# Performance work log

Hardware: AMD Instinct MI355X
Metric: run time of the kernel (lower is better)

## Reference

```python
import jax, jax.numpy as jnp
import numpy as np

HEAD_DIM = 256
L2_EPS = 1e-12  # tf.math.l2_normalize default epsilon


def setup_inputs() -> dict:
    key = jax.random.key(0)
    ks = jax.random.split(key, 6)
    B, U = 64, 2048
    D_dec, D_enc = 1024, 512
    H, K, A = 4, HEAD_DIM, 1024
    s = 0.075  # RandomUniform(-0.075, 0.075) kernel init
    return {
        "dec_state": jax.random.normal(ks[0], (B, D_dec), jnp.float32),
        "enc_state": jax.random.normal(ks[1], (B, U, D_enc), jnp.float32),
        "phi_w": jax.random.uniform(ks[2], (H, D_dec, K), jnp.float32, -s, s),
        "phi_b": jnp.zeros((H, K), jnp.float32),
        "psi_w": jax.random.uniform(ks[3], (H, D_enc, K), jnp.float32, -s, s),
        "psi_b": jnp.zeros((H, K), jnp.float32),
        "out_w": jax.random.uniform(ks[4], (H * D_enc, A), jnp.float32, -s, s),
        "out_b": jnp.zeros((A,), jnp.float32),
    }


def reference(dec_state, enc_state, phi_w, phi_b, psi_w, psi_b, out_w, out_b):
    B = dec_state.shape[0]
    # Per-head query/key projections, all heads at once.
    phi_s = jnp.einsum("bd,hdk->bhk", dec_state, phi_w) + phi_b[None]      # (B,H,K)
    psi_h = jnp.einsum("bue,hek->bhuk", enc_state, psi_w) + psi_b[None, :, None]  # (B,H,U,K)
    scale = 1.0 / jnp.sqrt(jnp.asarray(HEAD_DIM, jnp.float32))
    energy = jnp.einsum("bhk,bhuk->bhu", phi_s, psi_h) * scale              # (B,H,U)
    attn = jax.nn.softmax(energy, axis=-1)
    # NOTE: the original attends over the RAW enc_state (not psi_h).
    ctx = jnp.einsum("bhu,bue->bhe", attn, enc_state)                        # (B,H,E)
    # tf.math.l2_normalize over last axis
    sq = jnp.sum(ctx * ctx, axis=-1, keepdims=True)
    ctx = ctx * jax.lax.rsqrt(jnp.maximum(sq, L2_EPS))
    combined = ctx.reshape(B, -1)                                            # (B, H*E) == concat over heads
    return combined @ out_w + out_b
```

## Files before the change

kernel.cpp:

```cpp
#include <hip/hip_runtime.h>
#include <math.h>

typedef float f2 __attribute__((ext_vector_type(2)));

constexpr int NB = 64;
constexpr int NU = 2048;
constexpr int ND = 1024;
constexpr int NE = 512;
constexpr int NH = 4;
constexpr int NK = 256;
constexpr int NA = 1024;
constexpr int NS = 16;
constexpr int ROWS_PER_BLOCK = NU / NS;
constexpr int ROWS_PER_WAVE  = ROWS_PER_BLOCK / 4;
constexpr float SCALE = 0.0625f;

constexpr int RSPLIT = 16;
constexpr int RCH = (NH*NE)/RSPLIT;
constexpr int BT = 8;

constexpr int DSP = 16;

constexpr size_t WS_Q   = 0;
constexpr size_t WS_CTX = WS_Q + (size_t)NB*NH*NE;
constexpr size_t WS_P   = WS_CTX + (size_t)NB*NH*NE;

__global__ __launch_bounds__(256) void k_phi(
    const float* __restrict__ dec, const float* __restrict__ phi_w,
    float* __restrict__ P, float* __restrict__ q, float* __restrict__ ctxacc,
    const float* __restrict__ out_b, float* __restrict__ out)
{
  const int flat = blockIdx.x;
  const int kc = flat & 3;
  const int h  = (flat >> 2) & 3;
  const int ds = flat >> 4;
  const int t = threadIdx.x;

  ctxacc[(size_t)flat*512 + t]       = 0.f;
  ctxacc[(size_t)flat*512 + 256 + t] = 0.f;
  q[(size_t)flat*512 + t]            = 0.f;
  q[(size_t)flat*512 + 256 + t]      = 0.f;
  out[(size_t)flat*256 + t] = out_b[(flat*256 + t) & (NA-1)];

  const int d0 = ds*64, k0 = kc*64;

  __shared__ float phi_lds[64][64];
  __shared__ float dec_t[64][68];

  {
    const int kq = t & 15, r = t >> 4;
    const float* pwb = phi_w + ((size_t)h*ND + d0)*NK + k0;
    #pragma unroll
    for (int p = 0; p < 4; ++p) {
      float4 v = *(const float4*)(pwb + (size_t)(r + 16*p)*NK + 4*kq);
      *(float4*)&phi_lds[r + 16*p][4*kq] = v;
    }
    const float* db = dec + d0 + 4*kq;
    #pragma unroll
    for (int p = 0; p < 4; ++p) {
      const int b = r + 16*p;
      float4 v = *(const float4*)(db + (size_t)b*ND);
      dec_t[4*kq+0][b] = v.x; dec_t[4*kq+1][b] = v.y;
      dec_t[4*kq+2][b] = v.z; dec_t[4*kq+3][b] = v.w;
    }
  }
  __syncthreads();

  const int k = t & 63, bq = t >> 6, b0 = bq*16;
  f2 acc2[8];
  #pragma unroll
  for (int i = 0; i < 8; ++i) acc2[i] = f2{0.f, 0.f};
  #pragma unroll 4
  for (int d = 0; d < 64; ++d) {
    float w = phi_lds[d][k];
    f2 ww = f2{w, w};
    float4 a0 = *(const float4*)&dec_t[d][b0];
    float4 a1 = *(const float4*)&dec_t[d][b0+4];
    float4 a2 = *(const float4*)&dec_t[d][b0+8];
    float4 a3 = *(const float4*)&dec_t[d][b0+12];
    acc2[0] += f2{a0.x,a0.y}*ww; acc2[1] += f2{a0.z,a0.w}*ww;
    acc2[2] += f2{a1.x,a1.y}*ww; acc2[3] += f2{a1.z,a1.w}*ww;
    acc2[4] += f2{a2.x,a2.y}*ww; acc2[5] += f2{a2.z,a2.w}*ww;
    acc2[6] += f2{a3.x,a3.y}*ww; acc2[7] += f2{a3.z,a3.w}*ww;
  }
  float* pb = P + (((size_t)ds*64 + b0)*NH + h)*NK + k0 + k;
  #pragma unroll
  for (int j = 0; j < 8; ++j) {
    pb[(size_t)(2*j  )*NH*NK] = acc2[j][0];
    pb[(size_t)(2*j+1)*NH*NK] = acc2[j][1];
  }
}

__global__ __launch_bounds__(256) void k_q(
    const float* __restrict__ P, const float* __restrict__ phi_b,
    const float* __restrict__ psi_w, float* __restrict__ q)
{
  const int flat = blockIdx.x;
  const int ks = flat & 3;
  const int ec = (flat >> 2) & 7;
  const int h  = flat >> 5;
  const int t = threadIdx.x;
  const int k0 = ks*64, e0 = ec*64;

  __shared__ float phi_red[64][68];
  __shared__ float psi_lds[64][65];

  {
    const int e = t >> 2, kq4 = t & 3;
    const float* pb = psi_w + ((size_t)h*NE + e0 + e)*NK + k0 + 4*kq4;
    #pragma unroll
    for (int p = 0; p < 4; ++p) {
      float4 v = *(const float4*)(pb + 16*p);
      const int kk = 4*(kq4 + 4*p);
      psi_lds[e][kk+0] = v.x; psi_lds[e][kk+1] = v.y;
      psi_lds[e][kk+2] = v.z; psi_lds[e][kk+3] = v.w;
    }
  }
  {
    const int b = t >> 2, kq4 = t & 3;
    const float* pbase = P + ((size_t)b*NH + h)*NK + k0 + 4*kq4;
    #pragma unroll
    for (int p = 0; p < 4; ++p) {
      float4 s = make_float4(0.f, 0.f, 0.f, 0.f);
      #pragma unroll
      for (int dsi = 0; dsi < DSP; ++dsi) {
        float4 v = *(const float4*)(pbase + (size_t)dsi*64*NH*NK + 16*p);
        s.x += v.x; s.y += v.y; s.z += v.z; s.w += v.w;
      }
      const int kk = 4*(kq4 + 4*p);
      const float* bb = phi_b + h*NK + k0 + kk;
      phi_red[kk+0][b] = s.x + bb[0];
      phi_red[kk+1][b] = s.y + bb[1];
      phi_red[kk+2][b] = s.z + bb[2];
      phi_red[kk+3][b] = s.w + bb[3];
    }
  }
  __syncthreads();

  const int e = t & 63, bq = t >> 6, b0 = bq*16;
  f2 acc2[8];
  #pragma unroll
  for (int i = 0; i < 8; ++i) acc2[i] = f2{0.f, 0.f};
  #pragma unroll 4
  for (int kl = 0; kl < 64; ++kl) {
    float w = psi_lds[e][kl];
    f2 ww = f2{w, w};
    float4 a0 = *(const float4*)&phi_red[kl][b0];
    float4 a1 = *(const float4*)&phi_red[kl][b0+4];
    float4 a2 = *(const float4*)&phi_red[kl][b0+8];
    float4 a3 = *(const float4*)&phi_red[kl][b0+12];
    acc2[0] += f2{a0.x,a0.y}*ww; acc2[1] += f2{a0.z,a0.w}*ww;
    acc2[2] += f2{a1.x,a1.y}*ww; acc2[3] += f2{a1.z,a1.w}*ww;
    acc2[4] += f2{a2.x,a2.y}*ww; acc2[5] += f2{a2.z,a2.w}*ww;
    acc2[6] += f2{a3.x,a3.y}*ww; acc2[7] += f2{a3.z,a3.w}*ww;
  }
  float* qb = q + ((size_t)b0*NH + h)*NE + e0 + e;
  #pragma unroll
  for (int j = 0; j < 8; ++j) {
    unsafeAtomicAdd(qb + (size_t)(2*j  )*NH*NE, acc2[j][0]);
    unsafeAtomicAdd(qb + (size_t)(2*j+1)*NH*NE, acc2[j][1]);
  }
}

__device__ __forceinline__ f2 shflx(f2 v, int m) {
  return f2{__shfl_xor(v[0], m), __shfl_xor(v[1], m)};
}

__device__ __forceinline__ void fload(float4 (&r)[4], const float* myrow, int it) {
  const float* rp = myrow + (size_t)it*2*NE;
  r[0] = *(const float4*)(rp);
  r[1] = *(const float4*)(rp + 128);
  r[2] = *(const float4*)(rp + 256);
  r[3] = *(const float4*)(rp + 384);
}

__device__ __forceinline__ void fcomp(const float4 (&x)[4],
                                      const f2 (&qv)[NH][8], f2 (&acc2)[NH][8]) {
  f2 xf[8];
  xf[0]=f2{x[0].x,x[0].y}; xf[1]=f2{x[0].z,x[0].w};
  xf[2]=f2{x[1].x,x[1].y}; xf[3]=f2{x[1].z,x[1].w};
  xf[4]=f2{x[2].x,x[2].y}; xf[5]=f2{x[2].z,x[2].w};
  xf[6]=f2{x[3].x,x[3].y}; xf[7]=f2{x[3].z,x[3].w};
  f2 p[NH];
  #pragma unroll
  for (int h = 0; h < NH; ++h) {
    p[h] = xf[0]*qv[h][0];
    #pragma unroll
    for (int j = 1; j < 8; ++j) p[h] += xf[j]*qv[h][j];
  }
  f2 d01 = f2{p[0][0]+p[0][1], p[1][0]+p[1][1]};
  f2 d23 = f2{p[2][0]+p[2][1], p[3][0]+p[3][1]};
  #pragma unroll
  for (int off = 1; off < 32; off <<= 1) {
    d01 += shflx(d01, off);
    d23 += shflx(d23, off);
  }
  const float w[NH] = {__expf(d01[0]), __expf(d01[1]),
                       __expf(d23[0]), __expf(d23[1])};
  #pragma unroll
  for (int h = 0; h < NH; ++h) {
    f2 ww = f2{w[h], w[h]};
    #pragma unroll
    for (int j = 0; j < 8; ++j) acc2[h][j] += ww*xf[j];
  }
}

__global__ __launch_bounds__(256) void k_flash(
    const float* __restrict__ enc, const float* __restrict__ qg,
    float* __restrict__ ctxacc)
{
  const int s = blockIdx.x;
  const int b = blockIdx.y;
  const int t = threadIdx.x;
  const int wave = t >> 6;
  const int lane = t & 63;
  const int half = lane >> 5;
  const int l32 = lane & 31;

  f2 qv[NH][8];
  const float* qbase = qg + (size_t)b*NH*NE + 4*l32;
  #pragma unroll
  for (int h = 0; h < NH; ++h)
    #pragma unroll
    for (int ch = 0; ch < 4; ++ch) {
      float4 a = *(const float4*)(qbase + h*NE + ch*128);
      qv[h][2*ch]   = f2{a.x*SCALE, a.y*SCALE};
      qv[h][2*ch+1] = f2{a.z*SCALE, a.w*SCALE};
    }

  f2 acc2[NH][8];
  #pragma unroll
  for (int h = 0; h < NH; ++h)
    #pragma unroll
    for (int j = 0; j < 8; ++j) acc2[h][j] = f2{0.f, 0.f};

  const int u0 = s*ROWS_PER_BLOCK + wave*ROWS_PER_WAVE;
  const float* myrow = enc + ((size_t)b*NU + u0 + half)*NE + 4*l32;

  constexpr int NIT = ROWS_PER_WAVE/2;
  float4 R[4][4];
  #pragma unroll
  for (int c = 0; c < 4; ++c) fload(R[c], myrow, c);
  #pragma unroll
  for (int i = 0; i < NIT; ++i) {
    fcomp(R[i & 3], qv, acc2);
    if (i + 4 < NIT) fload(R[i & 3], myrow, i + 4);
  }

  #pragma unroll
  for (int h = 0; h < NH; ++h)
    #pragma unroll
    for (int j = 0; j < 8; ++j) acc2[h][j] += shflx(acc2[h][j], 32);

  __shared__ float acc_lds[4*NH*NE];
  if (half == 0) {
    #pragma unroll
    for (int h = 0; h < NH; ++h)
      #pragma unroll
      for (int ch = 0; ch < 4; ++ch)
        *(float4*)&acc_lds[(wave*NH + h)*NE + ch*128 + 4*l32] =
            make_float4(acc2[h][2*ch][0], acc2[h][2*ch][1],
                        acc2[h][2*ch+1][0], acc2[h][2*ch+1][1]);
  }
  __syncthreads();
  float* cb = ctxacc + (size_t)b*(NH*NE);
  #pragma unroll
  for (int h = 0; h < NH; ++h) {
    #pragma unroll
    for (int eo = 0; eo < 2; ++eo) {
      int e = t + eo*256;
      float v = acc_lds[(0*NH + h)*NE + e] + acc_lds[(1*NH + h)*NE + e]
              + acc_lds[(2*NH + h)*NE + e] + acc_lds[(3*NH + h)*NE + e];
      unsafeAtomicAdd(&cb[h*NE + e], v);
    }
  }
}

__global__ __launch_bounds__(256) void k_out(
    const float* __restrict__ ctxacc, const float* __restrict__ out_w,
    float* __restrict__ out)
{
  const int t = threadIdx.x;
  const int a = blockIdx.x*256 + t;
  const int b0 = blockIdx.y * BT;
  const int rc = blockIdx.z;
  const int h  = rc >> 2;
  const int e0 = (rc & 3) * RCH;

  __shared__ float rn_lds[BT];
  const int wv = t >> 6, lane = t & 63;
  {
    const int i = 2*wv + (lane >> 5);
    const int l32 = lane & 31;
    const float* row = ctxacc + (size_t)(b0+i)*(NH*NE) + (size_t)h*NE;
    float ss = 0.f;
    #pragma unroll
    for (int j = 0; j < 16; ++j) { float v = row[l32 + 32*j]; ss += v*v; }
    #pragma unroll
    for (int off = 1; off < 32; off <<= 1) ss += __shfl_xor(ss, off);
    if (l32 == 0) rn_lds[i] = rsqrtf(fmaxf(ss, 1e-12f));
  }
  __syncthreads();

  __shared__ float c_lds[RCH][BT];
  for (int g = t; g < RCH*BT; g += 256) {
    const int r = g & (RCH-1), i = g >> 7;
    c_lds[r][i] = ctxacc[(size_t)(b0+i)*(NH*NE) + (size_t)h*NE + e0 + r] * rn_lds[i];
  }
  __syncthreads();

  float accv[BT];
  #pragma unroll
  for (int i = 0; i < BT; ++i) accv[i] = 0.f;
  const float* w = out_w + ((size_t)rc*RCH)*NA + a;
  #pragma unroll 8
  for (int r = 0; r < RCH; ++r) {
    float wvv = w[(size_t)r*NA];
    float4 ca = *(const float4*)&c_lds[r][0];
    float4 cb = *(const float4*)&c_lds[r][4];
    accv[0] += ca.x*wvv; accv[1] += ca.y*wvv; accv[2] += ca.z*wvv; accv[3] += ca.w*wvv;
    accv[4] += cb.x*wvv; accv[5] += cb.y*wvv; accv[6] += cb.z*wvv; accv[7] += cb.w*wvv;
  }
  #pragma unroll
  for (int i = 0; i < BT; ++i)
    unsafeAtomicAdd(&out[(size_t)(b0+i)*NA + a], accv[i]);
}

extern "C" void kernel_launch(void* const* d_in, const int* in_sizes, int n_in,
                              void* d_out, int out_size, void* d_ws, size_t ws_size,
                              hipStream_t stream) {
  const float* dec   = (const float*)d_in[0];
  const float* enc   = (const float*)d_in[1];
  const float* phi_w = (const float*)d_in[2];
  const float* phi_b = (const float*)d_in[3];
  const float* psi_w = (const float*)d_in[4];
  const float* out_w = (const float*)d_in[6];
  const float* out_b = (const float*)d_in[7];
  float* out = (float*)d_out;
  float* ws = (float*)d_ws;
  float* q      = ws + WS_Q;
  float* ctxacc = ws + WS_CTX;
  float* P      = ws + WS_P;

  hipLaunchKernelGGL(k_phi,   dim3(NH*4*DSP),              dim3(256), 0, stream,
                     dec, phi_w, P, q, ctxacc, out_b, out);
  hipLaunchKernelGGL(k_q,     dim3(128),                   dim3(256), 0, stream,
                     P, phi_b, psi_w, q);
  hipLaunchKernelGGL(k_flash, dim3(NS, NB),                dim3(256), 0, stream,
                     enc, q, ctxacc);
  hipLaunchKernelGGL(k_out,   dim3(NA/256, NB/BT, RSPLIT), dim3(256), 0, stream,
                     ctxacc, out_w, out);
}
```

Before: 79.90 us.

## Stream encoder rows through LDS with async global_load_lds pipeline

Replaces the register-prefetch ring in the flash kernel with direct global-to-LDS async loads (global_load_lds) into a 4-slot per-wave shared buffer, waiting on vmcnt before reading each slot back into registers. The aim is to free the 64 prefetch registers to raise occupancy and to keep three row pairs in flight without spending VGPRs. The accumulation scratch now reuses the same shared buffer after a barrier. It adds an LDS round trip per element and a 64KB LDS footprint per block, which may itself limit occupancy. It also relies on hand-written vmcnt waits.

```diff
diff --git a/kernel.cpp b/kernel.cpp
--- a/kernel.cpp
+++ b/kernel.cpp
@@ -166,12 +166,13 @@
   return f2{__shfl_xor(v[0], m), __shfl_xor(v[1], m)};
 }
 
-__device__ __forceinline__ void fload(float4 (&r)[4], const float* myrow, int it) {
-  const float* rp = myrow + (size_t)it*2*NE;
-  r[0] = *(const float4*)(rp);
-  r[1] = *(const float4*)(rp + 128);
-  r[2] = *(const float4*)(rp + 256);
-  r[3] = *(const float4*)(rp + 384);
+__device__ __forceinline__ void waitv(int n) {
+  switch (n) {
+    case 0:  asm volatile("s_waitcnt vmcnt(0)"  ::: "memory"); break;
+    case 4:  asm volatile("s_waitcnt vmcnt(4)"  ::: "memory"); break;
+    case 8:  asm volatile("s_waitcnt vmcnt(8)"  ::: "memory"); break;
+    default: asm volatile("s_waitcnt vmcnt(12)" ::: "memory"); break;
+  }
 }
 
 __device__ __forceinline__ void fcomp(const float4 (&x)[4],
@@ -217,6 +218,8 @@
   const int half = lane >> 5;
   const int l32 = lane & 31;
 
+  __shared__ float sbuf[4][4][1024];
+
   f2 qv[NH][8];
   const float* qbase = qg + (size_t)b*NH*NE + 4*l32;
   #pragma unroll
@@ -235,16 +238,35 @@
     for (int j = 0; j < 8; ++j) acc2[h][j] = f2{0.f, 0.f};
 
   const int u0 = s*ROWS_PER_BLOCK + wave*ROWS_PER_WAVE;
-  const float* myrow = enc + ((size_t)b*NU + u0 + half)*NE + 4*l32;
+  const float* pairbase = enc + ((size_t)b*NU + u0)*NE;
+
+  auto STAGE = [&](int p, int sl) {
+    const float* src = pairbase + (size_t)p*1024 + 4*lane;
+    float* dst = &sbuf[wave][sl][0];
+    #pragma unroll
+    for (int j = 0; j < 4; ++j) {
+      __builtin_amdgcn_global_load_lds(
+          (const __attribute__((address_space(1))) void*)(src + j*256),
+          (__attribute__((address_space(3))) void*)(dst + j*256),
+          16, 0, 0);
+    }
+  };
 
   constexpr int NIT = ROWS_PER_WAVE/2;
-  float4 R[4][4];
-  #pragma unroll
-  for (int c = 0; c < 4; ++c) fload(R[c], myrow, c);
+  STAGE(0, 0); STAGE(1, 1); STAGE(2, 2);
   #pragma unroll
   for (int i = 0; i < NIT; ++i) {
-    fcomp(R[i & 3], qv, acc2);
-    if (i + 4 < NIT) fload(R[i & 3], myrow, i + 4);
+    if (i + 3 < NIT) STAGE(i + 3, (i + 3) & 3);
+    const int rem = (NIT - 1 - i < 3) ? (NIT - 1 - i) : 3;
+    waitv(4*rem);
+    __builtin_amdgcn_sched_barrier(0);
+    const float* sp = &sbuf[wave][i & 3][half*512 + 4*l32];
+    float4 x[4];
+    x[0] = *(const float4*)(sp);
+    x[1] = *(const float4*)(sp + 128);
+    x[2] = *(const float4*)(sp + 256);
+    x[3] = *(const float4*)(sp + 384);
+    fcomp(x, qv, acc2);
   }
 
   #pragma unroll
@@ -252,7 +274,8 @@
     #pragma unroll
     for (int j = 0; j < 8; ++j) acc2[h][j] += shflx(acc2[h][j], 32);
 
-  __shared__ float acc_lds[4*NH*NE];
+  __syncthreads();
+  float* acc_lds = &sbuf[0][0][0];
   if (half == 0) {
     #pragma unroll
     for (int h = 0; h < NH; ++h)
```

After: 84.23 us. 1.05x slower.
